# Performance work log

Measured on AMD Instinct MI355X. Metric: run time of the kernel, lower is better.

## Reference

```python
import jax, jax.numpy as jnp
import numpy as np

B = 524288   # batch rows
K = 8        # number of BooleanClassifiers
I = 64       # n_inputs
H = 32       # n_hidden
SCALE = 1.0  # LinearNetwork.scale (default [1.0])


def setup_inputs() -> dict:
    key = jax.random.key(0)
    k_x, k_w1, k_b1, k_w2, k_b2 = jax.random.split(key, 5)
    return {
        "x": jax.random.normal(k_x, (B, I), dtype=jnp.float32),
        "W1": jax.random.normal(k_w1, (K, H, I), dtype=jnp.float32) * 0.1,
        "b1": jax.random.normal(k_b1, (K, H), dtype=jnp.float32) * 0.1,
        "W2": jax.random.normal(k_w2, (K, H), dtype=jnp.float32) * 0.1,
        "b2": jax.random.normal(k_b2, (K,), dtype=jnp.float32) * 0.1,
        "bias": jnp.zeros((K,), dtype=jnp.float32),  # unused in training-mode forward
    }


def reference(x, W1, b1, W2, b2, bias):
    # Loop of K tiny Linear-Tanh-Linear-Tanh classifiers, fused as batched GEMMs.
    # h: [B, K, H]
    h = jnp.tanh(jnp.einsum("bi,khi->bkh", x, W1) + b1)
    # per-classifier scalar output, concatenated along dim=1 -> [B, K]
    out = jnp.tanh(jnp.einsum("bkh,kh->bk", h, W2) + b2)
    out = out * SCALE                   # LinearNetwork scale
    out = (out + 1.0) * 0.5 * SCALE     # LinearWithTanh training branch
    return out
```

## Files before the change

### kernel.cpp

```cpp
#include <hip/hip_runtime.h>

typedef __attribute__((ext_vector_type(8))) short short8;
typedef __attribute__((ext_vector_type(4))) float f32x4;

constexpr int B_ROWS   = 524288;
constexpr int ROWTILES = B_ROWS / 64;
constexpr int GRID     = 2048;
constexpr int ITERS    = ROWTILES / GRID;
constexpr float L2E2   = 2.8853900817779268f;

union V16 { uint4 u; short8 s; };

__device__ __forceinline__ unsigned pk(float lo, float hi) {
  const unsigned a = __float_as_uint(lo) + 0x8000u;
  const unsigned b = __float_as_uint(hi) + 0x8000u;
  return __builtin_amdgcn_perm(b, a, 0x07060302u);
}

__device__ __forceinline__ V16 pk8(f32x4 a, f32x4 b) {
  V16 v;
  v.u.x = pk(a[0], a[1]); v.u.y = pk(a[2], a[3]);
  v.u.z = pk(b[0], b[1]); v.u.w = pk(b[2], b[3]);
  return v;
}

__global__ __launch_bounds__(256, 4) void fused_mlp8(
    const float* __restrict__ x, const float* __restrict__ W1,
    const float* __restrict__ b1, const float* __restrict__ W2,
    const float* __restrict__ b2, float* __restrict__ out) {

  __shared__ V16 xb[2][512];

  const int tid  = threadIdx.x;
  const int wave = tid >> 6;
  const int lane = tid & 63;
  const int m16  = lane & 15;
  const int q    = lane >> 4;

  short8 w1f[4][2];
#pragma unroll
  for (int mt = 0; mt < 4; ++mt) {
    const int n = (wave * 4 + mt) * 16 + m16;
#pragma unroll
    for (int ks = 0; ks < 2; ++ks) {
      const float* p = W1 + n * 64 + ks * 32 + q * 8;
      const f32x4 u0 = *(const f32x4*)p, u1 = *(const f32x4*)(p + 4);
      f32x4 s0, s1;
#pragma unroll
      for (int r = 0; r < 4; ++r) { s0[r] = L2E2 * u0[r]; s1[r] = L2E2 * u1[r]; }
      w1f[mt][ks] = pk8(s0, s1).s;
    }
  }

  f32x4 kb1[4], w2m[4];
  float sw2[2] = {0.f, 0.f};
#pragma unroll
  for (int mt = 0; mt < 4; ++mt) {
    const int n0 = (wave * 4 + mt) * 16 + q * 4;
    const f32x4 b1x = *(const f32x4*)(b1 + n0);
    const f32x4 w2x = *(const f32x4*)(W2 + n0);
#pragma unroll
    for (int r = 0; r < 4; ++r) {
      kb1[mt][r] = L2E2 * b1x[r];
      w2m[mt][r] = -2.0f * w2x[r];
      sw2[mt >> 1] += w2x[r];
    }
  }
  float KSbn[2];
#pragma unroll
  for (int j = 0; j < 2; ++j) {
    float s = sw2[j];
    s += __shfl_xor(s, 16);
    s += __shfl_xor(s, 32);
    KSbn[j] = -L2E2 * (s + b2[wave * 2 + j]);
  }

  const int srow = tid >> 2;
  const int seg  = tid & 3;
  const int sw   = srow & 7;
  const float* gbase = x + (long)srow * 64 + seg * 16;

  f32x4 pf[4];
#pragma unroll
  for (int c = 0; c < 4; ++c)
    pf[c] = *(const f32x4*)(gbase + (long)blockIdx.x * 4096 + c * 4);
  xb[0][srow * 8 + ((seg * 2)     ^ sw)] = pk8(pf[0], pf[1]);
  xb[0][srow * 8 + ((seg * 2 + 1) ^ sw)] = pk8(pf[2], pf[3]);
#pragma unroll
  for (int c = 0; c < 4; ++c)
    pf[c] = *(const f32x4*)(gbase + ((long)blockIdx.x + GRID) * 4096 + c * 4);
  __syncthreads();

#pragma unroll
  for (int i = 0; i < ITERS; ++i) {
    const int p = i & 1;
    const long tile = (long)blockIdx.x + (long)i * GRID;
    const long obase = tile * 512 + wave * 2;

#pragma unroll
    for (int tt = 0; tt < 4; ++tt) {
      const int r   = tt * 16 + m16;
      const int rsw = r & 7;
      const short8 xf0 = xb[p][r * 8 + (q       ^ rsw)].s;
      const short8 xf1 = xb[p][r * 8 + ((q + 4) ^ rsw)].s;

      f32x4 acc[4];
#pragma unroll
      for (int mt = 0; mt < 4; ++mt) {
        f32x4 z = kb1[mt];
        z = __builtin_amdgcn_mfma_f32_16x16x32_bf16(w1f[mt][0], xf0, z, 0, 0, 0);
        z = __builtin_amdgcn_mfma_f32_16x16x32_bf16(w1f[mt][1], xf1, z, 0, 0, 0);
        acc[mt] = z;
      }

      float o0 = 0.f, o1 = 0.f;
#pragma unroll
      for (int j = 0; j < 2; ++j) {
        float P = 0.f;
#pragma unroll
        for (int t = 0; t < 2; ++t) {
          const int mt = j * 2 + t;
#pragma unroll
          for (int rr = 0; rr < 4; ++rr) {
            const float e = __builtin_amdgcn_exp2f(acc[mt][rr]);
            P = __builtin_fmaf(w2m[mt][rr], __builtin_amdgcn_rcpf(e + 1.0f), P);
          }
        }
        P += __shfl_xor(P, 16);
        P += __shfl_xor(P, 32);
        const float o = __builtin_amdgcn_rcpf(
            __builtin_amdgcn_exp2f(__builtin_fmaf(P, -L2E2, KSbn[j])) + 1.0f);
        if (j == 0) o0 = o; else o1 = o;
      }

      if (q == 0) {
        float2 st; st.x = o0; st.y = o1;
        *(float2*)(out + obase + (long)r * 8) = st;
      }
    }

    if (i + 1 < ITERS) {
      xb[p ^ 1][srow * 8 + ((seg * 2)     ^ sw)] = pk8(pf[0], pf[1]);
      xb[p ^ 1][srow * 8 + ((seg * 2 + 1) ^ sw)] = pk8(pf[2], pf[3]);
    }

    __syncthreads();

    if (i + 2 < ITERS) {
      const float* gp = gbase + (tile + 2 * GRID) * 4096;
#pragma unroll
      for (int c = 0; c < 4; ++c) pf[c] = *(const f32x4*)(gp + c * 4);
    }
  }
}

extern "C" void kernel_launch(void* const* d_in, const int* in_sizes, int n_in,
                              void* d_out, int out_size, void* d_ws, size_t ws_size,
                              hipStream_t stream) {
  const float* x  = (const float*)d_in[0];
  const float* W1 = (const float*)d_in[1];
  const float* b1 = (const float*)d_in[2];
  const float* W2 = (const float*)d_in[3];
  const float* b2 = (const float*)d_in[4];
  float* out = (float*)d_out;
  fused_mlp8<<<GRID, 256, 0, stream>>>(x, W1, b1, W2, b2, out);
}
```

Measured before the change: 208.8 us.

## Combine sigmoid reciprocals over a common denominator and drop the persistent tile loop

The hidden-layer sigmoid terms are now summed in groups of four over a common denominator. This replaces four reciprocals per group with one reciprocal plus a few multiplies, which lightens the transcendental-unit load that dominates the epilogue. The output bias and scale constants are folded into the accumulator's starting value, split across the four lanes that get summed. The persistent double-buffered loop is replaced by one 64-row tile per block on a larger grid, so overlap now comes from the hardware scheduler instead of software prefetch. The product of four (e+1) terms can overflow to inf when pre-activations are large, which could hurt accuracy.

```diff
diff --git a/kernel.cpp b/kernel.cpp
--- a/kernel.cpp
+++ b/kernel.cpp
@@ -3,11 +3,8 @@
 typedef __attribute__((ext_vector_type(8))) short short8;
 typedef __attribute__((ext_vector_type(4))) float f32x4;
 
-constexpr int B_ROWS   = 524288;
-constexpr int ROWTILES = B_ROWS / 64;
-constexpr int GRID     = 2048;
-constexpr int ITERS    = ROWTILES / GRID;
-constexpr float L2E2   = 2.8853900817779268f;
+constexpr int GRID  = 8192;
+constexpr float L2E2 = 2.8853900817779268f;
 
 union V16 { uint4 u; short8 s; };
 
@@ -29,13 +26,22 @@
     const float* __restrict__ b1, const float* __restrict__ W2,
     const float* __restrict__ b2, float* __restrict__ out) {
 
-  __shared__ V16 xb[2][512];
+  __shared__ V16 xb[512];
 
   const int tid  = threadIdx.x;
   const int wave = tid >> 6;
   const int lane = tid & 63;
   const int m16  = lane & 15;
   const int q    = lane >> 4;
+
+  const int srow = tid >> 2;
+  const int seg  = tid & 3;
+  const int sw   = srow & 7;
+  const float* gx = x + blockIdx.x * 4096 + srow * 64 + seg * 16;
+  const f32x4 pf0 = *(const f32x4*)gx;
+  const f32x4 pf1 = *(const f32x4*)(gx + 4);
+  const f32x4 pf2 = *(const f32x4*)(gx + 8);
+  const f32x4 pf3 = *(const f32x4*)(gx + 12);
 
   short8 w1f[4][2];
 #pragma unroll
@@ -52,7 +58,7 @@
     }
   }
 
-  f32x4 kb1[4], w2m[4];
+  f32x4 kb1[4], w2q[4];
   float sw2[2] = {0.f, 0.f};
 #pragma unroll
   for (int mt = 0; mt < 4; ++mt) {
@@ -62,7 +68,7 @@
 #pragma unroll
     for (int r = 0; r < 4; ++r) {
       kb1[mt][r] = L2E2 * b1x[r];
-      w2m[mt][r] = -2.0f * w2x[r];
+      w2q[mt][r] = (2.0f * L2E2) * w2x[r];
       sw2[mt >> 1] += w2x[r];
     }
   }
@@ -72,84 +78,60 @@
     float s = sw2[j];
     s += __shfl_xor(s, 16);
     s += __shfl_xor(s, 32);
-    KSbn[j] = -L2E2 * (s + b2[wave * 2 + j]);
+    KSbn[j] = -0.25f * L2E2 * (s + b2[wave * 2 + j]);
   }
 
-  const int srow = tid >> 2;
-  const int seg  = tid & 3;
-  const int sw   = srow & 7;
-  const float* gbase = x + (long)srow * 64 + seg * 16;
-
-  f32x4 pf[4];
-#pragma unroll
-  for (int c = 0; c < 4; ++c)
-    pf[c] = *(const f32x4*)(gbase + (long)blockIdx.x * 4096 + c * 4);
-  xb[0][srow * 8 + ((seg * 2)     ^ sw)] = pk8(pf[0], pf[1]);
-  xb[0][srow * 8 + ((seg * 2 + 1) ^ sw)] = pk8(pf[2], pf[3]);
-#pragma unroll
-  for (int c = 0; c < 4; ++c)
-    pf[c] = *(const f32x4*)(gbase + ((long)blockIdx.x + GRID) * 4096 + c * 4);
+  xb[srow * 8 + ((seg * 2)     ^ sw)] = pk8(pf0, pf1);
+  xb[srow * 8 + ((seg * 2 + 1) ^ sw)] = pk8(pf2, pf3);
   __syncthreads();
 
-#pragma unroll
-  for (int i = 0; i < ITERS; ++i) {
-    const int p = i & 1;
-    const long tile = (long)blockIdx.x + (long)i * GRID;
-    const long obase = tile * 512 + wave * 2;
+  const int obase = blockIdx.x * 512 + wave * 2;
 
 #pragma unroll
-    for (int tt = 0; tt < 4; ++tt) {
-      const int r   = tt * 16 + m16;
-      const int rsw = r & 7;
-      const short8 xf0 = xb[p][r * 8 + (q       ^ rsw)].s;
-      const short8 xf1 = xb[p][r * 8 + ((q + 4) ^ rsw)].s;
+  for (int tt = 0; tt < 4; ++tt) {
+    const int r   = tt * 16 + m16;
+    const int rsw = r & 7;
+    const short8 xf0 = xb[r * 8 + (q       ^ rsw)].s;
+    const short8 xf1 = xb[r * 8 + ((q + 4) ^ rsw)].s;
 
-      f32x4 acc[4];
+    f32x4 acc[4];
 #pragma unroll
-      for (int mt = 0; mt < 4; ++mt) {
-        f32x4 z = kb1[mt];
-        z = __builtin_amdgcn_mfma_f32_16x16x32_bf16(w1f[mt][0], xf0, z, 0, 0, 0);
-        z = __builtin_amdgcn_mfma_f32_16x16x32_bf16(w1f[mt][1], xf1, z, 0, 0, 0);
-        acc[mt] = z;
-      }
-
-      float o0 = 0.f, o1 = 0.f;
-#pragma unroll
-      for (int j = 0; j < 2; ++j) {
-        float P = 0.f;
-#pragma unroll
-        for (int t = 0; t < 2; ++t) {
-          const int mt = j * 2 + t;
-#pragma unroll
-          for (int rr = 0; rr < 4; ++rr) {
-            const float e = __builtin_amdgcn_exp2f(acc[mt][rr]);
-            P = __builtin_fmaf(w2m[mt][rr], __builtin_amdgcn_rcpf(e + 1.0f), P);
-          }
-        }
-        P += __shfl_xor(P, 16);
-        P += __shfl_xor(P, 32);
-        const float o = __builtin_amdgcn_rcpf(
-            __builtin_amdgcn_exp2f(__builtin_fmaf(P, -L2E2, KSbn[j])) + 1.0f);
-        if (j == 0) o0 = o; else o1 = o;
-      }
-
-      if (q == 0) {
-        float2 st; st.x = o0; st.y = o1;
-        *(float2*)(out + obase + (long)r * 8) = st;
-      }
+    for (int mt = 0; mt < 4; ++mt) {
+      f32x4 z = kb1[mt];
+      z = __builtin_amdgcn_mfma_f32_16x16x32_bf16(w1f[mt][0], xf0, z, 0, 0, 0);
+      z = __builtin_amdgcn_mfma_f32_16x16x32_bf16(w1f[mt][1], xf1, z, 0, 0, 0);
+      acc[mt] = z;
     }
 
-    if (i + 1 < ITERS) {
-      xb[p ^ 1][srow * 8 + ((seg * 2)     ^ sw)] = pk8(pf[0], pf[1]);
-      xb[p ^ 1][srow * 8 + ((seg * 2 + 1) ^ sw)] = pk8(pf[2], pf[3]);
+    float o0 = 0.f, o1 = 0.f;
+#pragma unroll
+    for (int j = 0; j < 2; ++j) {
+      float P = KSbn[j];
+#pragma unroll
+      for (int t = 0; t < 2; ++t) {
+        const int mt = j * 2 + t;
+        const float e0 = __builtin_amdgcn_exp2f(acc[mt][0]);
+        const float e1 = __builtin_amdgcn_exp2f(acc[mt][1]);
+        const float e2 = __builtin_amdgcn_exp2f(acc[mt][2]);
+        const float e3 = __builtin_amdgcn_exp2f(acc[mt][3]);
+        const float f0 = e0 + 1.0f, f1 = e1 + 1.0f;
+        const float f2 = e2 + 1.0f, f3 = e3 + 1.0f;
+        const float p01 = f0 * f1, p23 = f2 * f3;
+        const float n01 = __builtin_fmaf(w2q[mt][0], f1, w2q[mt][1] * f0);
+        const float n23 = __builtin_fmaf(w2q[mt][2], f3, w2q[mt][3] * f2);
+        const float N   = __builtin_fmaf(n01, p23, n23 * p01);
+        P = __builtin_fmaf(N, __builtin_amdgcn_rcpf(p01 * p23), P);
+      }
+      P += __shfl_xor(P, 16);
+      P += __shfl_xor(P, 32);
+      const float o = __builtin_amdgcn_rcpf(
+          __builtin_amdgcn_exp2f(P) + 1.0f);
+      if (j == 0) o0 = o; else o1 = o;
     }
 
-    __syncthreads();
-
-    if (i + 2 < ITERS) {
-      const float* gp = gbase + (tile + 2 * GRID) * 4096;
-#pragma unroll
-      for (int c = 0; c < 4; ++c) pf[c] = *(const f32x4*)(gp + c * 4);
+    if (q == 0) {
+      float2 st; st.x = o0; st.y = o1;
+      *(float2*)(out + obase + r * 8) = st;
     }
   }
 }
```

New measurement: 237.3 us. 13.7% more time.
